# Kernel optimization log

Hardware: AMD Instinct MI355X
Metric: run time of the kernel (lower is better)

Reference implementation:

```python
import jax, jax.numpy as jnp
import numpy as np

DIM = 1024
HEADS = 16
HEAD_DIM = DIM // HEADS
D_FF = 4 * DIM
EPS = 1e-5


def layer_norm(x, gamma, beta):
    mu = jnp.mean(x, axis=-1, keepdims=True)
    var = jnp.var(x, axis=-1, keepdims=True)
    return (x - mu) * jax.lax.rsqrt(var + EPS) * gamma + beta


def linear_attention(x, w_qkv, b_qkv, w_out, b_out):
    B, S, D = x.shape
    qkv = x @ w_qkv + b_qkv  # [B,S,3D]
    qkv = qkv.reshape(B, S, 3, HEADS, HEAD_DIM)
    q, k, v = qkv[:, :, 0], qkv[:, :, 1], qkv[:, :, 2]  # [B,S,H,Dh]
    q = jax.nn.softmax(q, axis=-1)       # feature-dim softmax
    k = jax.nn.softmax(k, axis=1)        # sequence-dim softmax
    kv = jnp.einsum('bshd,bshe->bhde', k, v)   # [B,H,Dh,Dh]
    out = jnp.einsum('bshd,bhde->bshe', q, kv)  # [B,S,H,Dh]
    out = out.reshape(B, S, D)
    return out @ w_out + b_out


def setup_inputs() -> dict:
    key = jax.random.key(0)
    ks = jax.random.split(key, 10)
    s = lambda fan_in: 1.0 / np.sqrt(fan_in)
    return {
        'x': jax.random.normal(ks[0], (4, 4096, DIM), dtype=jnp.float32),
        'w_qkv': jax.random.normal(ks[1], (DIM, 3 * DIM), jnp.float32) * s(DIM),
        'b_qkv': jnp.zeros((3 * DIM,), jnp.float32),
        'w_attn_out': jax.random.normal(ks[2], (DIM, DIM), jnp.float32) * s(DIM),
        'b_attn_out': jnp.zeros((DIM,), jnp.float32),
        'w_ffn1': jax.random.normal(ks[3], (DIM, D_FF), jnp.float32) * s(DIM),
        'b_ffn1': jnp.zeros((D_FF,), jnp.float32),
        'w_ffn2': jax.random.normal(ks[4], (D_FF, DIM), jnp.float32) * s(D_FF),
        'b_ffn2': jnp.zeros((DIM,), jnp.float32),
        'g1': jnp.ones((DIM,), jnp.float32),
        'beta1': jnp.zeros((DIM,), jnp.float32),
        'g2': jnp.ones((DIM,), jnp.float32),
        'beta2': jnp.zeros((DIM,), jnp.float32),
    }


def reference(x, w_qkv, b_qkv, w_attn_out, b_attn_out, w_ffn1, b_ffn1,
              w_ffn2, b_ffn2, g1, beta1, g2, beta2):
    # h = attn(norm1(x)); out = x + ffn(norm2(x + h))  (dropout=0)
    h = linear_attention(layer_norm(x, g1, beta1), w_qkv, b_qkv, w_attn_out, b_attn_out)
    z = layer_norm(x + h, g2, beta2)
    delta = jax.nn.gelu(z @ w_ffn1 + b_ffn1, approximate=False) @ w_ffn2 + b_ffn2
    return x + delta
```

## Files before the change

kernel.cpp:

```cpp
#include <hip/hip_runtime.h>
#include <hip/hip_bf16.h>
#include <cstdint>
#include <cstddef>

#define DIMC 1024
#define HEADS 16
#define HD 64
#define DFF 4096
#define BB 4
#define SS 4096
#define NROWS (BB*SS)

typedef __bf16 bf16_t;
typedef __bf16 bf16x8 __attribute__((ext_vector_type(8)));
typedef __bf16 bf16x4 __attribute__((ext_vector_type(4)));
typedef float  f32x4  __attribute__((ext_vector_type(4)));

#define GLDS16(gp, lp) \
  __builtin_amdgcn_global_load_lds((const __attribute__((address_space(1))) void*)(gp), \
                                   (__attribute__((address_space(3))) void*)(lp), 16, 0, 0)

#define MFMA16(a, b, c) __builtin_amdgcn_mfma_f32_16x16x32_bf16((a), (b), (c), 0, 0, 0)

__device__ __forceinline__ float fast_erf(float x) {
  float ax = fabsf(x);
  float t  = __builtin_amdgcn_rcpf(fmaf(0.3275911f, ax, 1.0f));
  float p  = t * fmaf(t, fmaf(t, fmaf(t, fmaf(t, 1.061405429f, -1.453152027f),
                                      1.421413741f), -0.284496736f), 0.254829592f);
  float er = 1.0f - p * __expf(-ax * ax);
  return copysignf(er, x);
}

__global__ __launch_bounds__(256) void prep_kernel(const float* __restrict__ w_qkv,
                                                   const float* __restrict__ w_out,
                                                   const float* __restrict__ w_ffn1,
                                                   const float* __restrict__ w_ffn2,
                                                   bf16_t* __restrict__ WT_QKV,
                                                   bf16_t* __restrict__ WT_OUT,
                                                   bf16_t* __restrict__ WT_FFN1,
                                                   bf16_t* __restrict__ WT_FFN2,
                                                   const float* __restrict__ x,
                                                   const float* __restrict__ gamma,
                                                   const float* __restrict__ beta,
                                                   bf16_t* __restrict__ act1) {
  const int bid = blockIdx.x;
  if (bid < 12288) {
    const float* W; bf16_t* Wt; int K, N, bx, by;
    if (bid < 3072)      { W = w_qkv;  Wt = WT_QKV;  K = 1024; N = 3072; bx = bid % 96;           by = bid / 96; }
    else if (bid < 4096) { W = w_out;  Wt = WT_OUT;  K = 1024; N = 1024; bx = (bid - 3072) % 32;  by = (bid - 3072) / 32; }
    else if (bid < 8192) { W = w_ffn1; Wt = WT_FFN1; K = 1024; N = 4096; bx = (bid - 4096) % 128; by = (bid - 4096) / 128; }
    else                 { W = w_ffn2; Wt = WT_FFN2; K = 4096; N = 1024; bx = (bid - 8192) % 32;  by = (bid - 8192) / 32; }
    __shared__ float tile[32][33];
    const int tx = threadIdx.x & 31, ty = threadIdx.x >> 5;
    const int c0 = bx * 32, r0 = by * 32;
    #pragma unroll
    for (int i = 0; i < 32; i += 8)
      tile[ty + i][tx] = W[(long)(r0 + ty + i) * N + c0 + tx];
    __syncthreads();
    #pragma unroll
    for (int i = 0; i < 32; i += 8)
      Wt[(long)(c0 + ty + i) * K + r0 + tx] = (bf16_t)tile[tx][ty + i];
  } else {
    long r = bid - 12288;
    int t = threadIdx.x;
    float4 v = ((const float4*)(x + r * DIMC))[t];
    float s  = v.x + v.y + v.z + v.w;
    float sq = v.x * v.x + v.y * v.y + v.z * v.z + v.w * v.w;
    #pragma unroll
    for (int o = 32; o > 0; o >>= 1) { s += __shfl_xor(s, o); sq += __shfl_xor(sq, o); }
    __shared__ float red[8];
    if ((t & 63) == 0) { red[(t >> 6) * 2] = s; red[(t >> 6) * 2 + 1] = sq; }
    __syncthreads();
    s  = red[0] + red[2] + red[4] + red[6];
    sq = red[1] + red[3] + red[5] + red[7];
    float mu  = s * (1.0f / DIMC);
    float var = sq * (1.0f / DIMC) - mu * mu;
    float rs  = 1.0f / sqrtf(var + 1e-5f);
    float4 g  = ((const float4*)gamma)[t];
    float4 bb = ((const float4*)beta)[t];
    bf16x4 o;
    o[0] = (bf16_t)((v.x - mu) * rs * g.x + bb.x);
    o[1] = (bf16_t)((v.y - mu) * rs * g.y + bb.y);
    o[2] = (bf16_t)((v.z - mu) * rs * g.z + bb.z);
    o[3] = (bf16_t)((v.w - mu) * rs * g.w + bb.w);
    ((bf16x4*)(act1 + r * DIMC))[t] = o;
  }
}

__global__ __launch_bounds__(256) void ln_kernel(const float* __restrict__ in,
                                                 const float* __restrict__ gamma,
                                                 const float* __restrict__ beta,
                                                 bf16_t* __restrict__ out) {
  long r = blockIdx.x;
  int t = threadIdx.x;
  float4 v = ((const float4*)(in + r * DIMC))[t];
  float s  = v.x + v.y + v.z + v.w;
  float sq = v.x * v.x + v.y * v.y + v.z * v.z + v.w * v.w;
  #pragma unroll
  for (int o = 32; o > 0; o >>= 1) { s += __shfl_xor(s, o); sq += __shfl_xor(sq, o); }
  __shared__ float red[8];
  if ((t & 63) == 0) { red[(t >> 6) * 2] = s; red[(t >> 6) * 2 + 1] = sq; }
  __syncthreads();
  s  = red[0] + red[2] + red[4] + red[6];
  sq = red[1] + red[3] + red[5] + red[7];
  float mu  = s * (1.0f / DIMC);
  float var = sq * (1.0f / DIMC) - mu * mu;
  float rs  = 1.0f / sqrtf(var + 1e-5f);
  float4 g  = ((const float4*)gamma)[t];
  float4 bb = ((const float4*)beta)[t];
  bf16x4 o;
  o[0] = (bf16_t)((v.x - mu) * rs * g.x + bb.x);
  o[1] = (bf16_t)((v.y - mu) * rs * g.y + bb.y);
  o[2] = (bf16_t)((v.z - mu) * rs * g.z + bb.z);
  o[3] = (bf16_t)((v.w - mu) * rs * g.w + bb.w);
  ((bf16x4*)(out + r * DIMC))[t] = o;
}

template <int MODE>
__global__ __launch_bounds__(256, 2) void gemm_bt(const bf16_t* __restrict__ A,
                                                  const bf16_t* __restrict__ Bt,
                                                  const float* __restrict__ bias,
                                                  const float* __restrict__ resid,
                                                  void* __restrict__ outp,
                                                  int M, int N, int K) {
  __shared__ bf16_t As[128 * 64];
  __shared__ bf16_t Bs[128 * 64];
  const int t = threadIdx.x;
  const int lane = t & 63;
  const int wave = t >> 6;

  const int nwg  = gridDim.x * gridDim.y;
  const int bid0 = blockIdx.y * gridDim.x + blockIdx.x;
  const int lg   = (bid0 & 7) * (nwg >> 3) + (bid0 >> 3);
  const int span = (int)gridDim.y << 2;
  const int gidx = lg / span;
  const int rem  = lg - gidx * span;
  const long arow0 = (long)(rem >> 2) * 128;
  const long brow0 = (long)((gidx << 2) + (rem & 3)) * 128;

  const int wm = (wave >> 1) * 64, wn = (wave & 1) * 64;

  f32x4 acc[4][4] = {};
  const int fr  = lane & 15;
  const int q4  = lane >> 4;
  const int frl = fr & 7;
  const int cr0 = ((q4    ) ^ frl) * 8;
  const int cr1 = ((q4 + 4) ^ frl) * 8;

  for (int kt = 0; kt < K; kt += 64) {
    #pragma unroll
    for (int p = 0; p < 4; ++p) {
      const int c = t + 256 * p;
      const int row = c >> 3;
      const int gch = ((c & 7) ^ (row & 7)) * 8;
      GLDS16(A  + (arow0 + row) * K + kt + gch, &As[c * 8]);
      GLDS16(Bt + (brow0 + row) * K + kt + gch, &Bs[c * 8]);
    }
    asm volatile("s_waitcnt vmcnt(0)" ::: "memory");
    __syncthreads();
    {
      bf16x8 a[4], b[4];
      #pragma unroll
      for (int i = 0; i < 4; ++i) {
        a[i] = *(const bf16x8*)&As[(wm + i * 16 + fr) * 64 + cr0];
        b[i] = *(const bf16x8*)&Bs[(wn + i * 16 + fr) * 64 + cr0];
      }
      #pragma unroll
      for (int i = 0; i < 4; ++i)
        #pragma unroll
        for (int j = 0; j < 4; ++j)
          acc[i][j] = MFMA16(a[i], b[j], acc[i][j]);
      #pragma unroll
      for (int i = 0; i < 4; ++i) {
        a[i] = *(const bf16x8*)&As[(wm + i * 16 + fr) * 64 + cr1];
        b[i] = *(const bf16x8*)&Bs[(wn + i * 16 + fr) * 64 + cr1];
      }
      #pragma unroll
      for (int i = 0; i < 4; ++i)
        #pragma unroll
        for (int j = 0; j < 4; ++j)
          acc[i][j] = MFMA16(a[i], b[j], acc[i][j]);
    }
    __syncthreads();
  }

  const int rq = q4 * 4;

  if (MODE == 3 && brow0 < 1024) {
    float bv[4];
    #pragma unroll
    for (int j = 0; j < 4; ++j) bv[j] = bias[brow0 + wn + j * 16 + fr];
    #pragma unroll
    for (int i = 0; i < 4; ++i) {
      #pragma unroll
      for (int r = 0; r < 4; ++r) {
        float v[4];
        #pragma unroll
        for (int j = 0; j < 4; ++j) v[j] = acc[i][j][r] + bv[j];
        float m = fmaxf(fmaxf(v[0], v[1]), fmaxf(v[2], v[3]));
        #pragma unroll
        for (int o = 1; o <= 8; o <<= 1) m = fmaxf(m, __shfl_xor(m, o));
        float e[4], s = 0.f;
        #pragma unroll
        for (int j = 0; j < 4; ++j) { e[j] = __expf(v[j] - m); s += e[j]; }
        #pragma unroll
        for (int o = 1; o <= 8; o <<= 1) s += __shfl_xor(s, o);
        float inv = 1.0f / s;
        long row = arow0 + wm + i * 16 + rq + r;
        #pragma unroll
        for (int j = 0; j < 4; ++j)
          ((bf16_t*)outp)[row * N + brow0 + wn + j * 16 + fr] = (bf16_t)(e[j] * inv);
      }
    }
  } else {
    #pragma unroll
    for (int i = 0; i < 4; ++i) {
      #pragma unroll
      for (int j = 0; j < 4; ++j) {
        long col = brow0 + wn + j * 16 + fr;
        float bv = bias[col];
        #pragma unroll
        for (int r = 0; r < 4; ++r) {
          long row = arow0 + wm + i * 16 + rq + r;
          float v = acc[i][j][r] + bv;
          if (MODE == 0 || MODE == 3) {
            ((bf16_t*)outp)[row * N + col] = (bf16_t)v;
          } else if (MODE == 1) {
            ((float*)outp)[row * N + col] = v + resid[row * N + col];
          } else {
            float g = 0.5f * v * (1.0f + fast_erf(v * 0.70710678118654752f));
            ((bf16_t*)outp)[row * N + col] = (bf16_t)g;
          }
        }
      }
    }
  }
}

__global__ __launch_bounds__(256) void kv_partial(const bf16_t* __restrict__ qkv,
                                                  float* __restrict__ kvp,
                                                  float* __restrict__ esump) {
  int bh = blockIdx.x, ch = blockIdx.y;
  int b = bh >> 4, h = bh & 15;
  int t = threadIdx.x;
  __shared__ float Kexp[64][65];
  __shared__ float Vs[64][66];
  int rowl = t >> 2, c0 = (t & 3) * 16;
  int dd = t >> 2, e0 = (t & 3) * 16;
  int lsq = (t & 3) * 16;
  float acc[16] = {};
  float esum = 0.f;
  for (int sb = 0; sb < 8; ++sb) {
    long s = (long)ch * 512 + sb * 64 + rowl;
    const bf16_t* base = qkv + ((long)b * SS + s) * 3072 + h * 64;
    bf16x8 k0 = *(const bf16x8*)(base + 1024 + c0);
    bf16x8 k1 = *(const bf16x8*)(base + 1024 + c0 + 8);
    bf16x8 v0 = *(const bf16x8*)(base + 2048 + c0);
    bf16x8 v1 = *(const bf16x8*)(base + 2048 + c0 + 8);
    __syncthreads();
    #pragma unroll
    for (int j = 0; j < 8; ++j) {
      Kexp[rowl][c0 + j]     = __expf((float)k0[j]);
      Kexp[rowl][c0 + 8 + j] = __expf((float)k1[j]);
      Vs[rowl][c0 + j]       = (float)v0[j];
      Vs[rowl][c0 + 8 + j]   = (float)v1[j];
    }
    __syncthreads();
    for (int ls = 0; ls < 64; ++ls) {
      float kd = Kexp[ls][dd];
      f32x4 va0 = *(const f32x4*)&Vs[ls][e0];
      f32x4 va1 = *(const f32x4*)&Vs[ls][e0 + 4];
      f32x4 va2 = *(const f32x4*)&Vs[ls][e0 + 8];
      f32x4 va3 = *(const f32x4*)&Vs[ls][e0 + 12];
      #pragma unroll
      for (int j = 0; j < 4; ++j) {
        acc[j]      += kd * va0[j];
        acc[j + 4]  += kd * va1[j];
        acc[j + 8]  += kd * va2[j];
        acc[j + 12] += kd * va3[j];
      }
    }
    #pragma unroll
    for (int l2 = 0; l2 < 16; ++l2) esum += Kexp[lsq + l2][dd];
  }
  float* dst = kvp + (long)(bh * 8 + ch) * 4096 + dd * 64 + e0;
  #pragma unroll
  for (int j = 0; j < 16; ++j) dst[j] = acc[j];
  esum += __shfl_xor(esum, 1);
  esum += __shfl_xor(esum, 2);
  if ((t & 3) == 0) esump[(long)(bh * 8 + ch) * 64 + dd] = esum;
}

__global__ void kv_reduce(const float* __restrict__ kvp, const float* __restrict__ esump,
                          bf16_t* __restrict__ kvT) {
  int bh = blockIdx.x, t = threadIdx.x;
  __shared__ float ei[64];
  if (t < 64) {
    float es = 0.f;
    #pragma unroll
    for (int c = 0; c < 8; ++c) es += esump[(long)(bh * 8 + c) * 64 + t];
    ei[t] = 1.0f / es;
  }
  __syncthreads();
  for (int p = t; p < 4096; p += 256) {
    int d = p >> 6, e = p & 63;
    float s = 0.f;
    #pragma unroll
    for (int c = 0; c < 8; ++c) s += kvp[(long)(bh * 8 + c) * 4096 + p];
    kvT[(long)bh * 4096 + e * 64 + d] = (bf16_t)(s * ei[d]);
  }
}

__global__ __launch_bounds__(256) void attn_apply(const bf16_t* __restrict__ qkv,
                                                  const bf16_t* __restrict__ kvT,
                                                  bf16_t* __restrict__ attn) {
  int bh = blockIdx.x, sc = blockIdx.y;
  int b = bh >> 4, h = bh & 15;
  int t = threadIdx.x, lane = t & 63, w = t >> 6;
  __shared__ bf16_t kvs[64 * 64];
  for (int i = t * 8; i < 4096; i += 256 * 8)
    *(bf16x8*)&kvs[i] = *(const bf16x8*)(kvT + (long)bh * 4096 + i);
  __syncthreads();
  int fr = lane & 15, kq = (lane >> 4) * 8;
  long qrow = (long)b * SS + sc * 128 + w * 32;
  f32x4 acc[2][4] = {};
  #pragma unroll
  for (int kk = 0; kk < 2; ++kk) {
    bf16x8 a0 = *(const bf16x8*)(qkv + (qrow + fr) * 3072      + h * 64 + kk * 32 + kq);
    bf16x8 a1 = *(const bf16x8*)(qkv + (qrow + 16 + fr) * 3072 + h * 64 + kk * 32 + kq);
    #pragma unroll
    for (int j = 0; j < 4; ++j) {
      bf16x8 bfr = *(const bf16x8*)&kvs[(j * 16 + fr) * 64 + kk * 32 + kq];
      acc[0][j] = MFMA16(a0, bfr, acc[0][j]);
      acc[1][j] = MFMA16(a1, bfr, acc[1][j]);
    }
  }
  int rq = (lane >> 4) * 4;
  #pragma unroll
  for (int i = 0; i < 2; ++i)
    #pragma unroll
    for (int j = 0; j < 4; ++j)
      #pragma unroll
      for (int r = 0; r < 4; ++r)
        attn[(qrow + i * 16 + rq + r) * 1024 + h * 64 + j * 16 + fr] = (bf16_t)acc[i][j][r];
}

extern "C" void kernel_launch(void* const* d_in, const int* in_sizes, int n_in,
                              void* d_out, int out_size, void* d_ws, size_t ws_size,
                              hipStream_t stream) {
  (void)in_sizes; (void)n_in; (void)out_size;
  const float* x      = (const float*)d_in[0];
  const float* w_qkv  = (const float*)d_in[1];
  const float* b_qkv  = (const float*)d_in[2];
  const float* w_out  = (const float*)d_in[3];
  const float* b_out  = (const float*)d_in[4];
  const float* w_ffn1 = (const float*)d_in[5];
  const float* b_ffn1 = (const float*)d_in[6];
  const float* w_ffn2 = (const float*)d_in[7];
  const float* b_ffn2 = (const float*)d_in[8];
  const float* g1     = (const float*)d_in[9];
  const float* be1    = (const float*)d_in[10];
  const float* g2     = (const float*)d_in[11];
  const float* be2    = (const float*)d_in[12];

  char* ws = (char*)d_ws;
  constexpr size_t WT_QKV_OFF  = 0;
  constexpr size_t WT_OUT_OFF  = WT_QKV_OFF  + 6291456;
  constexpr size_t WT_FFN1_OFF = WT_OUT_OFF  + 2097152;
  constexpr size_t WT_FFN2_OFF = WT_FFN1_OFF + 8388608;
  constexpr size_t ESUMP_OFF   = WT_FFN2_OFF + 8388608;
  constexpr size_t KVP_OFF     = ESUMP_OFF   + 294912;
  constexpr size_t KVT_OFF     = KVP_OFF     + 8388608;
  constexpr size_t ACT1_OFF    = KVT_OFF     + 524288;
  constexpr size_t BIG_OFF     = ACT1_OFF    + 33554432;

  bf16_t* WT_QKV  = (bf16_t*)(ws + WT_QKV_OFF);
  bf16_t* WT_OUT  = (bf16_t*)(ws + WT_OUT_OFF);
  bf16_t* WT_FFN1 = (bf16_t*)(ws + WT_FFN1_OFF);
  bf16_t* WT_FFN2 = (bf16_t*)(ws + WT_FFN2_OFF);
  float*  ESUMP   = (float*) (ws + ESUMP_OFF);
  float*  KVP     = (float*) (ws + KVP_OFF);
  bf16_t* KVT     = (bf16_t*)(ws + KVT_OFF);
  bf16_t* ACT1    = (bf16_t*)(ws + ACT1_OFF);
  bf16_t* QKV     = (bf16_t*)(ws + BIG_OFF);
  bf16_t* GACT    = (bf16_t*)(ws + BIG_OFF);
  float*  Y       = (float*)  d_out;

  const bool big_ws = ws_size >= (size_t)(BIG_OFF + 134217728ull);

  prep_kernel<<<12288 + NROWS, 256, 0, stream>>>(w_qkv, w_out, w_ffn1, w_ffn2,
                                                 WT_QKV, WT_OUT, WT_FFN1, WT_FFN2,
                                                 x, g1, be1, ACT1);

  gemm_bt<3><<<dim3(3072 / 128, NROWS / 128), 256, 0, stream>>>(ACT1, WT_QKV, b_qkv, nullptr, QKV, NROWS, 3072, 1024);

  kv_partial<<<dim3(64, 8), 256, 0, stream>>>(QKV, KVP, ESUMP);
  kv_reduce<<<64, 256, 0, stream>>>(KVP, ESUMP, KVT);
  attn_apply<<<dim3(64, SS / 128), 256, 0, stream>>>(QKV, KVT, ACT1);

  gemm_bt<1><<<dim3(1024 / 128, NROWS / 128), 256, 0, stream>>>(ACT1, WT_OUT, b_out, x, Y, NROWS, 1024, 1024);

  ln_kernel<<<NROWS, 256, 0, stream>>>(Y, g2, be2, ACT1);

  if (big_ws) {
    gemm_bt<2><<<dim3(4096 / 128, NROWS / 128), 256, 0, stream>>>(ACT1, WT_FFN1, b_ffn1, nullptr, GACT, NROWS, 4096, 1024);
    gemm_bt<1><<<dim3(1024 / 128, NROWS / 128), 256, 0, stream>>>(GACT, WT_FFN2, b_ffn2, x, (float*)d_out, NROWS, 1024, 4096);
  } else {
    for (int c = 0; c < 2; ++c) {
      const long r0 = (long)c * 8192;
      gemm_bt<2><<<dim3(4096 / 128, 8192 / 128), 256, 0, stream>>>(
          ACT1 + r0 * 1024, WT_FFN1, b_ffn1, nullptr, GACT, 8192, 4096, 1024);
      gemm_bt<1><<<dim3(1024 / 128, 8192 / 128), 256, 0, stream>>>(
          GACT, WT_FFN2, b_ffn2, x + r0 * 1024, (float*)d_out + r0 * 1024, 8192, 1024, 4096);
    }
  }
}
```

Baseline: 634.4 us.

## Fold normalized KV into output projection and store pre-LN residual in bf16

Each per-head KV matrix is premultiplied with the matching slice of W_out, giving a per-batch projection matrix. The out-projection GEMM then reads softmaxed Q straight from the QKV buffer (lda 3072, per-batch B stride), so the attn_apply kernel and its intermediate activation round-trip go away. The residual sum before the second layer norm is now written as bf16 into the output buffer instead of fp32, which halves that traffic for both the write and the LN read. In exchange there is a small extra kv_wout kernel and an 8 MB per-batch matrix, plus some bf16 rounding loss in the pre-LN residual.

```diff
diff --git a/kernel.cpp b/kernel.cpp
--- a/kernel.cpp
+++ b/kernel.cpp
@@ -87,15 +87,16 @@
   }
 }
 
-__global__ __launch_bounds__(256) void ln_kernel(const float* __restrict__ in,
-                                                 const float* __restrict__ gamma,
-                                                 const float* __restrict__ beta,
-                                                 bf16_t* __restrict__ out) {
+__global__ __launch_bounds__(256) void ln_bf16(const bf16_t* __restrict__ in,
+                                               const float* __restrict__ gamma,
+                                               const float* __restrict__ beta,
+                                               bf16_t* __restrict__ out) {
   long r = blockIdx.x;
   int t = threadIdx.x;
-  float4 v = ((const float4*)(in + r * DIMC))[t];
-  float s  = v.x + v.y + v.z + v.w;
-  float sq = v.x * v.x + v.y * v.y + v.z * v.z + v.w * v.w;
+  bf16x4 v4 = ((const bf16x4*)(in + r * DIMC))[t];
+  float v0 = v4[0], v1 = v4[1], v2 = v4[2], v3 = v4[3];
+  float s  = v0 + v1 + v2 + v3;
+  float sq = v0 * v0 + v1 * v1 + v2 * v2 + v3 * v3;
   #pragma unroll
   for (int o = 32; o > 0; o >>= 1) { s += __shfl_xor(s, o); sq += __shfl_xor(sq, o); }
   __shared__ float red[8];
@@ -109,10 +110,10 @@
   float4 g  = ((const float4*)gamma)[t];
   float4 bb = ((const float4*)beta)[t];
   bf16x4 o;
-  o[0] = (bf16_t)((v.x - mu) * rs * g.x + bb.x);
-  o[1] = (bf16_t)((v.y - mu) * rs * g.y + bb.y);
-  o[2] = (bf16_t)((v.z - mu) * rs * g.z + bb.z);
-  o[3] = (bf16_t)((v.w - mu) * rs * g.w + bb.w);
+  o[0] = (bf16_t)((v0 - mu) * rs * g.x + bb.x);
+  o[1] = (bf16_t)((v1 - mu) * rs * g.y + bb.y);
+  o[2] = (bf16_t)((v2 - mu) * rs * g.z + bb.z);
+  o[3] = (bf16_t)((v3 - mu) * rs * g.w + bb.w);
   ((bf16x4*)(out + r * DIMC))[t] = o;
 }
 
@@ -122,7 +123,7 @@
                                                   const float* __restrict__ bias,
                                                   const float* __restrict__ resid,
                                                   void* __restrict__ outp,
-                                                  int M, int N, int K) {
+                                                  int M, int N, int K, int lda, long bstride) {
   __shared__ bf16_t As[128 * 64];
   __shared__ bf16_t Bs[128 * 64];
   const int t = threadIdx.x;
@@ -138,6 +139,8 @@
   const long arow0 = (long)(rem >> 2) * 128;
   const long brow0 = (long)((gidx << 2) + (rem & 3)) * 128;
 
+  const bf16_t* BtB = Bt + (arow0 >> 12) * bstride;
+
   const int wm = (wave >> 1) * 64, wn = (wave & 1) * 64;
 
   f32x4 acc[4][4] = {};
@@ -153,8 +156,8 @@
       const int c = t + 256 * p;
       const int row = c >> 3;
       const int gch = ((c & 7) ^ (row & 7)) * 8;
-      GLDS16(A  + (arow0 + row) * K + kt + gch, &As[c * 8]);
-      GLDS16(Bt + (brow0 + row) * K + kt + gch, &Bs[c * 8]);
+      GLDS16(A   + (arow0 + row) * (long)lda + kt + gch, &As[c * 8]);
+      GLDS16(BtB + (brow0 + row) * (long)K   + kt + gch, &Bs[c * 8]);
     }
     asm volatile("s_waitcnt vmcnt(0)" ::: "memory");
     __syncthreads();
@@ -227,6 +230,8 @@
             ((bf16_t*)outp)[row * N + col] = (bf16_t)v;
           } else if (MODE == 1) {
             ((float*)outp)[row * N + col] = v + resid[row * N + col];
+          } else if (MODE == 4) {
+            ((bf16_t*)outp)[row * N + col] = (bf16_t)(v + resid[row * N + col]);
           } else {
             float g = 0.5f * v * (1.0f + fast_erf(v * 0.70710678118654752f));
             ((bf16_t*)outp)[row * N + col] = (bf16_t)g;
@@ -292,7 +297,7 @@
 }
 
 __global__ void kv_reduce(const float* __restrict__ kvp, const float* __restrict__ esump,
-                          bf16_t* __restrict__ kvT) {
+                          bf16_t* __restrict__ kvN) {
   int bh = blockIdx.x, t = threadIdx.x;
   __shared__ float ei[64];
   if (t < 64) {
@@ -303,46 +308,76 @@
   }
   __syncthreads();
   for (int p = t; p < 4096; p += 256) {
-    int d = p >> 6, e = p & 63;
+    int d = p >> 6;
     float s = 0.f;
     #pragma unroll
     for (int c = 0; c < 8; ++c) s += kvp[(long)(bh * 8 + c) * 4096 + p];
-    kvT[(long)bh * 4096 + e * 64 + d] = (bf16_t)(s * ei[d]);
-  }
-}
-
-__global__ __launch_bounds__(256) void attn_apply(const bf16_t* __restrict__ qkv,
-                                                  const bf16_t* __restrict__ kvT,
-                                                  bf16_t* __restrict__ attn) {
-  int bh = blockIdx.x, sc = blockIdx.y;
-  int b = bh >> 4, h = bh & 15;
-  int t = threadIdx.x, lane = t & 63, w = t >> 6;
-  __shared__ bf16_t kvs[64 * 64];
-  for (int i = t * 8; i < 4096; i += 256 * 8)
-    *(bf16x8*)&kvs[i] = *(const bf16x8*)(kvT + (long)bh * 4096 + i);
+    kvN[(long)bh * 4096 + p] = (bf16_t)(s * ei[d]);
+  }
+}
+
+__global__ __launch_bounds__(256) void kv_wout(const bf16_t* __restrict__ kvN,
+                                               const bf16_t* __restrict__ WT_OUT,
+                                               bf16_t* __restrict__ MBT) {
+  const int jt = blockIdx.x;
+  const int bh = blockIdx.y;
+  const int b  = bh >> 4, h = bh & 15;
+  const int t = threadIdx.x, lane = t & 63, wave = t >> 6;
+  __shared__ bf16_t Ws[256 * 64];
+  __shared__ bf16_t Ks[64 * 64];
+  const int fr = lane & 15, q4 = lane >> 4, frl = fr & 7;
+  const int cr0 = ((q4    ) ^ frl) * 8;
+  const int cr1 = ((q4 + 4) ^ frl) * 8;
+  #pragma unroll
+  for (int p = 0; p < 8; ++p) {
+    const int c = t + 256 * p;
+    const int row = c >> 3;
+    const int gch = ((c & 7) ^ (row & 7)) * 8;
+    GLDS16(WT_OUT + (long)(jt * 256 + row) * 1024 + h * 64 + gch, &Ws[c * 8]);
+  }
+  #pragma unroll
+  for (int p = 0; p < 2; ++p) {
+    const int c = t + 256 * p;
+    const int row = c >> 3;
+    const int gch = ((c & 7) ^ (row & 7)) * 8;
+    GLDS16(kvN + (long)bh * 4096 + row * 64 + gch, &Ks[c * 8]);
+  }
+  asm volatile("s_waitcnt vmcnt(0)" ::: "memory");
   __syncthreads();
-  int fr = lane & 15, kq = (lane >> 4) * 8;
-  long qrow = (long)b * SS + sc * 128 + w * 32;
-  f32x4 acc[2][4] = {};
+  f32x4 acc[4][4] = {};
+  const int wj = wave * 64;
+  {
+    bf16x8 a[4], bfr[4];
+    #pragma unroll
+    for (int i = 0; i < 4; ++i) {
+      a[i]   = *(const bf16x8*)&Ws[(wj + i * 16 + fr) * 64 + cr0];
+      bfr[i] = *(const bf16x8*)&Ks[(i * 16 + fr) * 64 + cr0];
+    }
+    #pragma unroll
+    for (int i = 0; i < 4; ++i)
+      #pragma unroll
+      for (int j = 0; j < 4; ++j)
+        acc[i][j] = MFMA16(a[i], bfr[j], acc[i][j]);
+    #pragma unroll
+    for (int i = 0; i < 4; ++i) {
+      a[i]   = *(const bf16x8*)&Ws[(wj + i * 16 + fr) * 64 + cr1];
+      bfr[i] = *(const bf16x8*)&Ks[(i * 16 + fr) * 64 + cr1];
+    }
+    #pragma unroll
+    for (int i = 0; i < 4; ++i)
+      #pragma unroll
+      for (int j = 0; j < 4; ++j)
+        acc[i][j] = MFMA16(a[i], bfr[j], acc[i][j]);
+  }
+  const int rq = q4 * 4;
   #pragma unroll
-  for (int kk = 0; kk < 2; ++kk) {
-    bf16x8 a0 = *(const bf16x8*)(qkv + (qrow + fr) * 3072      + h * 64 + kk * 32 + kq);
-    bf16x8 a1 = *(const bf16x8*)(qkv + (qrow + 16 + fr) * 3072 + h * 64 + kk * 32 + kq);
-    #pragma unroll
-    for (int j = 0; j < 4; ++j) {
-      bf16x8 bfr = *(const bf16x8*)&kvs[(j * 16 + fr) * 64 + kk * 32 + kq];
-      acc[0][j] = MFMA16(a0, bfr, acc[0][j]);
-      acc[1][j] = MFMA16(a1, bfr, acc[1][j]);
-    }
-  }
-  int rq = (lane >> 4) * 4;
-  #pragma unroll
-  for (int i = 0; i < 2; ++i)
+  for (int i = 0; i < 4; ++i)
     #pragma unroll
     for (int j = 0; j < 4; ++j)
       #pragma unroll
       for (int r = 0; r < 4; ++r)
-        attn[(qrow + i * 16 + rq + r) * 1024 + h * 64 + j * 16 + fr] = (bf16_t)acc[i][j][r];
+        MBT[((long)b * 1024 + jt * 256 + wj + i * 16 + rq + r) * 1024 + h * 64 + j * 16 + fr]
+            = (bf16_t)acc[i][j][r];
 }
 
 extern "C" void kernel_launch(void* const* d_in, const int* in_sizes, int n_in,
@@ -370,8 +405,9 @@
   constexpr size_t WT_FFN2_OFF = WT_FFN1_OFF + 8388608;
   constexpr size_t ESUMP_OFF   = WT_FFN2_OFF + 8388608;
   constexpr size_t KVP_OFF     = ESUMP_OFF   + 294912;
-  constexpr size_t KVT_OFF     = KVP_OFF     + 8388608;
-  constexpr size_t ACT1_OFF    = KVT_OFF     + 524288;
+  constexpr size_t KVN_OFF     = KVP_OFF     + 8388608;
+  constexpr size_t MBT_OFF     = KVN_OFF     + 524288;
+  constexpr size_t ACT1_OFF    = MBT_OFF     + 8388608;
   constexpr size_t BIG_OFF     = ACT1_OFF    + 33554432;
 
   bf16_t* WT_QKV  = (bf16_t*)(ws + WT_QKV_OFF);
@@ -380,11 +416,12 @@
   bf16_t* WT_FFN2 = (bf16_t*)(ws + WT_FFN2_OFF);
   float*  ESUMP   = (float*) (ws + ESUMP_OFF);
   float*  KVP     = (float*) (ws + KVP_OFF);
-  bf16_t* KVT     = (bf16_t*)(ws + KVT_OFF);
+  bf16_t* KVN     = (bf16_t*)(ws + KVN_OFF);
+  bf16_t* MBT     = (bf16_t*)(ws + MBT_OFF);
   bf16_t* ACT1    = (bf16_t*)(ws + ACT1_OFF);
   bf16_t* QKV     = (bf16_t*)(ws + BIG_OFF);
   bf16_t* GACT    = (bf16_t*)(ws + BIG_OFF);
-  float*  Y       = (float*)  d_out;
+  bf16_t* YB      = (bf16_t*)d_out;
 
   const bool big_ws = ws_size >= (size_t)(BIG_OFF + 134217728ull);
 
@@ -392,26 +429,30 @@
                                                  WT_QKV, WT_OUT, WT_FFN1, WT_FFN2,
                                                  x, g1, be1, ACT1);
 
-  gemm_bt<3><<<dim3(3072 / 128, NROWS / 128), 256, 0, stream>>>(ACT1, WT_QKV, b_qkv, nullptr, QKV, NROWS, 3072, 1024);
+  gemm_bt<3><<<dim3(3072 / 128, NROWS / 128), 256, 0, stream>>>(ACT1, WT_QKV, b_qkv, nullptr, QKV,
+                                                                NROWS, 3072, 1024, 1024, 0);
 
   kv_partial<<<dim3(64, 8), 256, 0, stream>>>(QKV, KVP, ESUMP);
-  kv_reduce<<<64, 256, 0, stream>>>(KVP, ESUMP, KVT);
-  attn_apply<<<dim3(64, SS / 128), 256, 0, stream>>>(QKV, KVT, ACT1);
-
-  gemm_bt<1><<<dim3(1024 / 128, NROWS / 128), 256, 0, stream>>>(ACT1, WT_OUT, b_out, x, Y, NROWS, 1024, 1024);
-
-  ln_kernel<<<NROWS, 256, 0, stream>>>(Y, g2, be2, ACT1);
+  kv_reduce<<<64, 256, 0, stream>>>(KVP, ESUMP, KVN);
+  kv_wout<<<dim3(4, 64), 256, 0, stream>>>(KVN, WT_OUT, MBT);
+
+  gemm_bt<4><<<dim3(1024 / 128, NROWS / 128), 256, 0, stream>>>(QKV, MBT, b_out, x, YB,
+                                                                NROWS, 1024, 1024, 3072, 1048576);
+
+  ln_bf16<<<NROWS, 256, 0, stream>>>(YB, g2, be2, ACT1);
 
   if (big_ws) {
-    gemm_bt<2><<<dim3(4096 / 128, NROWS / 128), 256, 0, stream>>>(ACT1, WT_FFN1, b_ffn1, nullptr, GACT, NROWS, 4096, 1024);
-    gemm_bt<1><<<dim3(1024 / 128, NROWS / 128), 256, 0, stream>>>(GACT, WT_FFN2, b_ffn2, x, (float*)d_out, NROWS, 1024, 4096);
+    gemm_bt<2><<<dim3(4096 / 128, NROWS / 128), 256, 0, stream>>>(ACT1, WT_FFN1, b_ffn1, nullptr, GACT,
+                                                                  NROWS, 4096, 1024, 1024, 0);
+    gemm_bt<1><<<dim3(1024 / 128, NROWS / 128), 256, 0, stream>>>(GACT, WT_FFN2, b_ffn2, x, (float*)d_out,
+                                                                  NROWS, 1024, 4096, 4096, 0);
   } else {
     for (int c = 0; c < 2; ++c) {
       const long r0 = (long)c * 8192;
       gemm_bt<2><<<dim3(4096 / 128, 8192 / 128), 256, 0, stream>>>(
-          ACT1 + r0 * 1024, WT_FFN1, b_ffn1, nullptr, GACT, 8192, 4096, 1024);
+          ACT1 + r0 * 1024, WT_FFN1, b_ffn1, nullptr, GACT, 8192, 4096, 1024, 1024, 0);
       gemm_bt<1><<<dim3(1024 / 128, 8192 / 128), 256, 0, stream>>>(
-          GACT, WT_FFN2, b_ffn2, x + r0 * 1024, (float*)d_out + r0 * 1024, 8192, 1024, 4096);
-    }
-  }
-}
+          GACT, WT_FFN2, b_ffn2, x + r0 * 1024, (float*)d_out + r0 * 1024, 8192, 1024, 4096, 4096, 0);
+    }
+  }
+}
```

Measured after the change: 606.6 us. 4.4% less time.
